# Kernel tuning notes

Measured on AMD Instinct MI355X. Metric: run time of the kernel, lower is better.

## Reference

```python
import jax, jax.numpy as jnp
import numpy as np

D = 256          # in_dim == out_dim for both layers
B, S = 8, 1024   # batch, seq_len
EPS = 1e-5       # LayerNorm eps (torch default)


def _layernorm(x, g, b):
    mu = jnp.mean(x, axis=-1, keepdims=True)
    var = jnp.var(x, axis=-1, keepdims=True)
    return (x - mu) * jax.lax.rsqrt(var + EPS) * g + b


def _periods(d):
    i = jnp.arange(d, dtype=jnp.float32)
    # periods[i, j] = i*d + j + 2
    return i[:, None] * d + i[None, :] + 2.0


def _layer(x, M, P, g, b, positions):
    # x: [B, S, in_dim] -> [B, S, out_dim]
    x_trans = jnp.einsum('bsj,ij->bsi', x, M)      # x @ M.T
    x_trans = _layernorm(x_trans, g, b)
    k = positions.astype(jnp.float32)[:, None, None]            # [S,1,1]
    phi = jnp.cos(2.0 * jnp.pi * k / _periods(D)[None])         # [S,D,D]
    Mk = P[None] * phi                                          # [S,D,D]
    Nk = jnp.einsum('bsj,sij->bsi', x_trans, Mk)
    # use_residual='separate' with in_dim==out_dim -> Identity residual
    return Nk + x


def setup_inputs() -> dict:
    key = jax.random.key(0)
    ks = jax.random.split(key, 5)
    seq = jax.random.normal(ks[0], (B, S, D), dtype=jnp.float32)
    M1 = jax.random.uniform(ks[1], (D, D), jnp.float32, -0.5, 0.5)
    P1 = jax.random.uniform(ks[2], (D, D), jnp.float32, -0.1, 0.1)
    M2 = jax.random.uniform(ks[3], (D, D), jnp.float32, -0.5, 0.5)
    P2 = jax.random.uniform(ks[4], (D, D), jnp.float32, -0.1, 0.1)
    g1 = jnp.ones((D,), jnp.float32); b1 = jnp.zeros((D,), jnp.float32)
    g2 = jnp.ones((D,), jnp.float32); b2 = jnp.zeros((D,), jnp.float32)
    return {"seq": seq, "M1": M1, "P1": P1, "g1": g1, "b1": b1,
            "M2": M2, "P2": P2, "g2": g2, "b2": b2}


def reference(seq, M1, P1, g1, b1, M2, P2, g2, b2):
    positions = jnp.arange(S)
    x = _layer(seq, M1, P1, g1, b1, positions)
    x = _layer(x, M2, P2, g2, b2, positions)
    return x
```

## Files before the change

kernel.cpp:

```cpp
#include <hip/hip_runtime.h>

#define DD 256
#define BB 8
#define SS 1024
#define XSTRIDE 264

#define LAYER_BYTES 524288
#define PTAB_OFF    131072
#define ITAB_OFF    262144
#define WS_NEEDED   (2 * LAYER_BYTES)

typedef _Float16 half8  __attribute__((ext_vector_type(8)));
typedef _Float16 half2t __attribute__((ext_vector_type(2)));
typedef __fp16   fp16x2 __attribute__((ext_vector_type(2)));
typedef __attribute__((ext_vector_type(4))) float float4v;

__device__ __forceinline__ half2t pkrtz(float a, float b) {
    union { fp16x2 f; half2t h; } cv;
    cv.f = __builtin_amdgcn_cvt_pkrtz(a, b);
    return cv.h;
}

__global__ void build_tabs(const float* __restrict__ M1, const float* __restrict__ P1,
                           const float* __restrict__ M2, const float* __restrict__ P2,
                           char* __restrict__ ws)
{
    int gid   = blockIdx.x * 256 + threadIdx.x;
    int layer = gid >> 13;
    int gi    = gid & 8191;
    int idx   = gi >> 6;
    int lane  = gi & 63;
    int kt    = idx >> 4;
    int wt    = idx & 15;
    int l15   = lane & 15, quad = lane >> 4;
    int n     = 16 * wt + l15;
    int j0    = kt * 32 + quad * 8;

    const float* Msrc = layer ? M2 : M1;
    const float* Psrc = layer ? P2 : P1;

    union { half8 h; half2t h2[4]; } mh, ph;
    float iv[8];
    #pragma unroll
    for (int e = 0; e < 4; ++e) {
        float ma = Msrc[(size_t)n * DD + j0 + 2 * e];
        float mb = Msrc[(size_t)n * DD + j0 + 2 * e + 1];
        float pa = Psrc[(size_t)n * DD + j0 + 2 * e];
        float pb = Psrc[(size_t)n * DD + j0 + 2 * e + 1];
        mh.h2[e] = pkrtz(ma, mb);
        ph.h2[e] = pkrtz(pa, pb);
        iv[2 * e]     = 1.0f / (float)(n * DD + j0 + 2 * e + 2);
        iv[2 * e + 1] = 1.0f / (float)(n * DD + j0 + 2 * e + 3);
    }
    char* base = ws + (size_t)layer * LAYER_BYTES;
    ((half8*)base)[gi]                       = mh.h;
    ((half8*)(base + PTAB_OFF))[gi]          = ph.h;
    float4* it = (float4*)(base + ITAB_OFF);
    it[2 * gi]     = make_float4(iv[0], iv[1], iv[2], iv[3]);
    it[2 * gi + 1] = make_float4(iv[4], iv[5], iv[6], iv[7]);
}

template<bool TABS>
__global__ __launch_bounds__(512, 4)
void fused_hierddpm(const float* __restrict__ seq,
                    const float* __restrict__ M1, const float* __restrict__ P1,
                    const float* __restrict__ g1, const float* __restrict__ be1,
                    const float* __restrict__ M2, const float* __restrict__ P2,
                    const float* __restrict__ g2, const float* __restrict__ be2,
                    const char* __restrict__ ws,
                    float* __restrict__ out)
{
    __shared__ __align__(16) _Float16 xsb[16][XSTRIDE];
    __shared__ __align__(16) _Float16 xtb[16][XSTRIDE];
    __shared__ float stats[8][16][2];

    const int tid  = threadIdx.x;
    const int w    = tid >> 6;
    const int lane = tid & 63;
    const int l15  = lane & 15;
    const int quad = lane >> 4;
    const int s0   = blockIdx.x * 2;
    const float k0 = (float)s0, k1 = (float)(s0 + 1);

    {
        const float4* seq4 = (const float4*)seq;
        #pragma unroll
        for (int u = 0; u < 2; ++u) {
            int v  = tid + 512 * u;
            int sl = v >> 9;
            int rm = v & 511;
            int b  = rm >> 6, j4 = rm & 63;
            float4 x = seq4[((size_t)b * SS + s0 + sl) * 64 + j4];
            half2t* dst = (half2t*)&xsb[sl * 8 + b][4 * j4];
            dst[0] = pkrtz(x.x, x.y);
            dst[1] = pkrtz(x.z, x.w);
        }
    }

    float res[2][4];
    {
        const int sl = quad >> 1;
        #pragma unroll
        for (int t = 0; t < 2; ++t) {
            int col = 16 * (2 * w + t) + l15;
            #pragma unroll
            for (int reg = 0; reg < 4; ++reg) {
                int b = (quad * 4 + reg) & 7;
                res[t][reg] = seq[((size_t)b * SS + s0 + sl) * DD + col];
            }
        }
    }
    __syncthreads();

    #pragma unroll 1
    for (int layer = 0; layer < 2; ++layer) {
        const float* M  = layer ? M2  : M1;
        const float* P  = layer ? P2  : P1;
        const float* g  = layer ? g2  : g1;
        const float* be = layer ? be2 : be1;
        const char*  lbase = ws + (size_t)layer * LAYER_BYTES;
        const half8*  Mtab = (const half8*)lbase;
        const half8*  Ptab = (const half8*)(lbase + PTAB_OFF);
        const float4* Itab = (const float4*)(lbase + ITAB_OFF);

        float4v acc1[2];
        acc1[0] = (float4v){0.f, 0.f, 0.f, 0.f};
        acc1[1] = (float4v){0.f, 0.f, 0.f, 0.f};

        #pragma unroll 1
        for (int kt = 0; kt < 8; ++kt) {
            half8 a = *(const half8*)&xsb[l15][kt * 32 + quad * 8];
            #pragma unroll
            for (int t = 0; t < 2; ++t) {
                half8 bfrag;
                if (TABS) {
                    bfrag = Mtab[(kt * 16 + 2 * w + t) * 64 + lane];
                } else {
                    int n = 16 * (2 * w + t) + l15;
                    const float4* Mr = (const float4*)M +
                        ((size_t)n * 64 + kt * 8 + quad * 2);
                    float4 m0 = Mr[0], m1 = Mr[1];
                    union { half8 h; half2t h2[4]; } bb;
                    bb.h2[0] = pkrtz(m0.x, m0.y);
                    bb.h2[1] = pkrtz(m0.z, m0.w);
                    bb.h2[2] = pkrtz(m1.x, m1.y);
                    bb.h2[3] = pkrtz(m1.z, m1.w);
                    bfrag = bb.h;
                }
                acc1[t] = __builtin_amdgcn_mfma_f32_16x16x32_f16(a, bfrag, acc1[t], 0, 0, 0);
            }
        }

        {
            #pragma unroll
            for (int reg = 0; reg < 4; ++reg) {
                float sm = acc1[0][reg] + acc1[1][reg];
                float sq = fmaf(acc1[0][reg], acc1[0][reg], acc1[1][reg] * acc1[1][reg]);
                #pragma unroll
                for (int off = 1; off < 16; off <<= 1) {
                    sm += __shfl_xor(sm, off, 64);
                    sq += __shfl_xor(sq, off, 64);
                }
                if (l15 == 0) {
                    stats[w][quad * 4 + reg][0] = sm;
                    stats[w][quad * 4 + reg][1] = sq;
                }
            }
        }
        __syncthreads();
        {
            float mu[4], rs[4];
            #pragma unroll
            for (int reg = 0; reg < 4; ++reg) {
                int m = quad * 4 + reg;
                float sm = 0.f, sq = 0.f;
                #pragma unroll
                for (int ww = 0; ww < 8; ++ww) {
                    sm += stats[ww][m][0];
                    sq += stats[ww][m][1];
                }
                float mm = sm * (1.f / DD);
                mu[reg] = mm;
                rs[reg] = rsqrtf(sq * (1.f / DD) - mm * mm + 1e-5f);
            }
            #pragma unroll
            for (int t = 0; t < 2; ++t) {
                int col = 16 * (2 * w + t) + l15;
                float gv = g[col], bv = be[col];
                #pragma unroll
                for (int reg = 0; reg < 4; ++reg) {
                    float v = fmaf((acc1[t][reg] - mu[reg]) * rs[reg], gv, bv);
                    xtb[quad * 4 + reg][col] = (_Float16)v;
                }
            }
        }
        __syncthreads();

        float4v accS[2][2];
        #pragma unroll
        for (int sl = 0; sl < 2; ++sl)
            #pragma unroll
            for (int t = 0; t < 2; ++t) accS[sl][t] = (float4v){0.f, 0.f, 0.f, 0.f};

        #pragma unroll 2
        for (int kt = 0; kt < 8; ++kt) {
            half8 a = *(const half8*)&xtb[l15][kt * 32 + quad * 8];
            #pragma unroll
            for (int t = 0; t < 2; ++t) {
                union { half8 h; half2t h2[4]; } pv;
                float iv[8];
                if (TABS) {
                    int gi = (kt * 16 + 2 * w + t) * 64 + lane;
                    pv.h = Ptab[gi];
                    float4 i0 = Itab[2 * gi], i1 = Itab[2 * gi + 1];
                    iv[0] = i0.x; iv[1] = i0.y; iv[2] = i0.z; iv[3] = i0.w;
                    iv[4] = i1.x; iv[5] = i1.y; iv[6] = i1.z; iv[7] = i1.w;
                } else {
                    int n = 16 * (2 * w + t) + l15;
                    const float4* Pr = (const float4*)P +
                        ((size_t)n * 64 + kt * 8 + quad * 2);
                    float4 p0 = Pr[0], p1 = Pr[1];
                    pv.h2[0] = pkrtz(p0.x, p0.y);
                    pv.h2[1] = pkrtz(p0.z, p0.w);
                    pv.h2[2] = pkrtz(p1.x, p1.y);
                    pv.h2[3] = pkrtz(p1.z, p1.w);
                    float pbase = (float)(n * DD + kt * 32 + quad * 8 + 2);
                    #pragma unroll
                    for (int e = 0; e < 8; ++e)
                        iv[e] = __builtin_amdgcn_rcpf(pbase + (float)e);
                }
                union { half8 h; half2t h2[4]; } b0, b1;
                #pragma unroll
                for (int e = 0; e < 4; ++e) {
                    float ia = iv[2 * e], ib = iv[2 * e + 1];
                    half2t c0 = pkrtz(
                        __builtin_amdgcn_cosf(__builtin_amdgcn_fractf(k0 * ia)),
                        __builtin_amdgcn_cosf(__builtin_amdgcn_fractf(k0 * ib)));
                    half2t c1 = pkrtz(
                        __builtin_amdgcn_cosf(__builtin_amdgcn_fractf(k1 * ia)),
                        __builtin_amdgcn_cosf(__builtin_amdgcn_fractf(k1 * ib)));
                    b0.h2[e] = pv.h2[e] * c0;
                    b1.h2[e] = pv.h2[e] * c1;
                }
                accS[0][t] = __builtin_amdgcn_mfma_f32_16x16x32_f16(a, b0.h, accS[0][t], 0, 0, 0);
                accS[1][t] = __builtin_amdgcn_mfma_f32_16x16x32_f16(a, b1.h, accS[1][t], 0, 0, 0);
            }
        }

        #pragma unroll
        for (int t = 0; t < 2; ++t) {
            int col = 16 * (2 * w + t) + l15;
            float4v av = (quad < 2) ? accS[0][t] : accS[1][t];
            int sl = quad >> 1;
            #pragma unroll
            for (int reg = 0; reg < 4; ++reg) {
                int m = quad * 4 + reg;
                int b = m & 7;
                float val = av[reg] + res[t][reg];
                if (layer == 0) {
                    res[t][reg] = val;
                    xsb[m][col] = (_Float16)val;
                } else {
                    out[((size_t)b * SS + s0 + sl) * DD + col] = val;
                }
            }
        }
        if (layer == 0) __syncthreads();
    }
}

extern "C" void kernel_launch(void* const* d_in, const int* in_sizes, int n_in,
                              void* d_out, int out_size, void* d_ws, size_t ws_size,
                              hipStream_t stream)
{
    const float* seq = (const float*)d_in[0];
    const float* M1  = (const float*)d_in[1];
    const float* P1  = (const float*)d_in[2];
    const float* g1  = (const float*)d_in[3];
    const float* b1  = (const float*)d_in[4];
    const float* M2  = (const float*)d_in[5];
    const float* P2  = (const float*)d_in[6];
    const float* g2  = (const float*)d_in[7];
    const float* b2  = (const float*)d_in[8];
    float* out = (float*)d_out;

    if (ws_size >= WS_NEEDED) {
        build_tabs<<<64, 256, 0, stream>>>(M1, P1, M2, P2, (char*)d_ws);
        fused_hierddpm<true><<<SS / 2, 512, 0, stream>>>(
            seq, M1, P1, g1, b1, M2, P2, g2, b2, (const char*)d_ws, out);
    } else {
        fused_hierddpm<false><<<SS / 2, 512, 0, stream>>>(
            seq, M1, P1, g1, b1, M2, P2, g2, b2, nullptr, out);
    }
}
```

Before: 114.4 us.

## Replace per-element cosines with second-order angle-difference expansion from one sincos

```diff
diff --git a/kernel.cpp b/kernel.cpp
--- a/kernel.cpp
+++ b/kernel.cpp
@@ -7,8 +7,11 @@
 
 #define LAYER_BYTES 524288
 #define PTAB_OFF    131072
-#define ITAB_OFF    262144
+#define JTAB_OFF    262144
 #define WS_NEEDED   (2 * LAYER_BYTES)
+
+#define TWO_PI 6.28318530717958647692f
+#define PBMIN  640.0f
 
 typedef _Float16 half8  __attribute__((ext_vector_type(8)));
 typedef _Float16 half2t __attribute__((ext_vector_type(2)));
@@ -40,24 +43,26 @@
     const float* Psrc = layer ? P2 : P1;
 
     union { half8 h; half2t h2[4]; } mh, ph;
-    float iv[8];
     #pragma unroll
     for (int e = 0; e < 4; ++e) {
-        float ma = Msrc[(size_t)n * DD + j0 + 2 * e];
-        float mb = Msrc[(size_t)n * DD + j0 + 2 * e + 1];
-        float pa = Psrc[(size_t)n * DD + j0 + 2 * e];
-        float pb = Psrc[(size_t)n * DD + j0 + 2 * e + 1];
-        mh.h2[e] = pkrtz(ma, mb);
-        ph.h2[e] = pkrtz(pa, pb);
-        iv[2 * e]     = 1.0f / (float)(n * DD + j0 + 2 * e + 2);
-        iv[2 * e + 1] = 1.0f / (float)(n * DD + j0 + 2 * e + 3);
-    }
+        mh.h2[e] = pkrtz(Msrc[(size_t)n * DD + j0 + 2 * e],
+                         Msrc[(size_t)n * DD + j0 + 2 * e + 1]);
+        ph.h2[e] = pkrtz(Psrc[(size_t)n * DD + j0 + 2 * e],
+                         Psrc[(size_t)n * DD + j0 + 2 * e + 1]);
+    }
+    float p0 = (float)(n * DD + j0 + 2);
+    float dv[8];
+    dv[0] = 1.0f / p0;
+    #pragma unroll
+    for (int e = 1; e < 8; ++e)
+        dv[e] = TWO_PI * (float)e / (p0 * (p0 + (float)e));
+
     char* base = ws + (size_t)layer * LAYER_BYTES;
-    ((half8*)base)[gi]                       = mh.h;
-    ((half8*)(base + PTAB_OFF))[gi]          = ph.h;
-    float4* it = (float4*)(base + ITAB_OFF);
-    it[2 * gi]     = make_float4(iv[0], iv[1], iv[2], iv[3]);
-    it[2 * gi + 1] = make_float4(iv[4], iv[5], iv[6], iv[7]);
+    ((half8*)base)[gi]              = mh.h;
+    ((half8*)(base + PTAB_OFF))[gi] = ph.h;
+    float4* jt = (float4*)(base + JTAB_OFF);
+    jt[2 * gi]     = make_float4(dv[0], dv[1], dv[2], dv[3]);
+    jt[2 * gi + 1] = make_float4(dv[4], dv[5], dv[6], dv[7]);
 }
 
 template<bool TABS>
@@ -121,13 +126,13 @@
         const char*  lbase = ws + (size_t)layer * LAYER_BYTES;
         const half8*  Mtab = (const half8*)lbase;
         const half8*  Ptab = (const half8*)(lbase + PTAB_OFF);
-        const float4* Itab = (const float4*)(lbase + ITAB_OFF);
+        const float4* Jtab = (const float4*)(lbase + JTAB_OFF);
 
         float4v acc1[2];
         acc1[0] = (float4v){0.f, 0.f, 0.f, 0.f};
         acc1[1] = (float4v){0.f, 0.f, 0.f, 0.f};
 
-        #pragma unroll 1
+        #pragma unroll 2
         for (int kt = 0; kt < 8; ++kt) {
             half8 a = *(const half8*)&xsb[l15][kt * 32 + quad * 8];
             #pragma unroll
@@ -207,40 +212,61 @@
             half8 a = *(const half8*)&xtb[l15][kt * 32 + quad * 8];
             #pragma unroll
             for (int t = 0; t < 2; ++t) {
-                union { half8 h; half2t h2[4]; } pv;
-                float iv[8];
+                const int n = 16 * (2 * w + t) + l15;
+                const float p0f = (float)(n * DD + kt * 32 + quad * 8 + 2);
+                union { half8 h; half2t h2[4]; } pv, b0, b1;
+
                 if (TABS) {
                     int gi = (kt * 16 + 2 * w + t) * 64 + lane;
                     pv.h = Ptab[gi];
-                    float4 i0 = Itab[2 * gi], i1 = Itab[2 * gi + 1];
-                    iv[0] = i0.x; iv[1] = i0.y; iv[2] = i0.z; iv[3] = i0.w;
-                    iv[4] = i1.x; iv[5] = i1.y; iv[6] = i1.z; iv[7] = i1.w;
+                    float4 ja = Jtab[2 * gi], jb = Jtab[2 * gi + 1];
+                    const float iv0 = ja.x;
+                    float f0 = __builtin_amdgcn_fractf(k0 * iv0);
+                    float c0 = __builtin_amdgcn_cosf(f0);
+                    float s0v = __builtin_amdgcn_sinf(f0);
+                    float dl = TWO_PI * iv0;
+                    float c1 = fmaf(-dl, fmaf(0.5f * dl, c0, s0v), c0);
+                    float s1v = fmaf(dl, fmaf(-0.5f * dl, s0v, c0), s0v);
+                    const float dd[8] = {0.f, ja.y, ja.z, ja.w, jb.x, jb.y, jb.z, jb.w};
+                    #pragma unroll
+                    for (int ep = 0; ep < 4; ++ep) {
+                        float da = dd[2 * ep], db = dd[2 * ep + 1];
+                        float pa0 = k0 * da, pb0 = k0 * db;
+                        float ce0a = fmaf(pa0, fmaf(-0.5f * pa0, c0, s0v), c0);
+                        float ce0b = fmaf(pb0, fmaf(-0.5f * pb0, c0, s0v), c0);
+                        float pa1 = k1 * da, pb1 = k1 * db;
+                        float ce1a = fmaf(pa1, fmaf(-0.5f * pa1, c1, s1v), c1);
+                        float ce1b = fmaf(pb1, fmaf(-0.5f * pb1, c1, s1v), c1);
+                        if (p0f < PBMIN) {
+                            float ia = __builtin_amdgcn_rcpf(p0f + (float)(2 * ep));
+                            float ib = __builtin_amdgcn_rcpf(p0f + (float)(2 * ep + 1));
+                            ce0a = __builtin_amdgcn_cosf(__builtin_amdgcn_fractf(k0 * ia));
+                            ce0b = __builtin_amdgcn_cosf(__builtin_amdgcn_fractf(k0 * ib));
+                            ce1a = __builtin_amdgcn_cosf(__builtin_amdgcn_fractf(k1 * ia));
+                            ce1b = __builtin_amdgcn_cosf(__builtin_amdgcn_fractf(k1 * ib));
+                        }
+                        b0.h2[ep] = pv.h2[ep] * pkrtz(ce0a, ce0b);
+                        b1.h2[ep] = pv.h2[ep] * pkrtz(ce1a, ce1b);
+                    }
                 } else {
-                    int n = 16 * (2 * w + t) + l15;
                     const float4* Pr = (const float4*)P +
                         ((size_t)n * 64 + kt * 8 + quad * 2);
-                    float4 p0 = Pr[0], p1 = Pr[1];
-                    pv.h2[0] = pkrtz(p0.x, p0.y);
-                    pv.h2[1] = pkrtz(p0.z, p0.w);
-                    pv.h2[2] = pkrtz(p1.x, p1.y);
-                    pv.h2[3] = pkrtz(p1.z, p1.w);
-                    float pbase = (float)(n * DD + kt * 32 + quad * 8 + 2);
+                    float4 q0 = Pr[0], q1 = Pr[1];
+                    pv.h2[0] = pkrtz(q0.x, q0.y);
+                    pv.h2[1] = pkrtz(q0.z, q0.w);
+                    pv.h2[2] = pkrtz(q1.x, q1.y);
+                    pv.h2[3] = pkrtz(q1.z, q1.w);
                     #pragma unroll
-                    for (int e = 0; e < 8; ++e)
-                        iv[e] = __builtin_amdgcn_rcpf(pbase + (float)e);
-                }
-                union { half8 h; half2t h2[4]; } b0, b1;
-                #pragma unroll
-                for (int e = 0; e < 4; ++e) {
-                    float ia = iv[2 * e], ib = iv[2 * e + 1];
-                    half2t c0 = pkrtz(
-                        __builtin_amdgcn_cosf(__builtin_amdgcn_fractf(k0 * ia)),
-                        __builtin_amdgcn_cosf(__builtin_amdgcn_fractf(k0 * ib)));
-                    half2t c1 = pkrtz(
-                        __builtin_amdgcn_cosf(__builtin_amdgcn_fractf(k1 * ia)),
-                        __builtin_amdgcn_cosf(__builtin_amdgcn_fractf(k1 * ib)));
-                    b0.h2[e] = pv.h2[e] * c0;
-                    b1.h2[e] = pv.h2[e] * c1;
+                    for (int ep = 0; ep < 4; ++ep) {
+                        float ia = __builtin_amdgcn_rcpf(p0f + (float)(2 * ep));
+                        float ib = __builtin_amdgcn_rcpf(p0f + (float)(2 * ep + 1));
+                        float ce0a = __builtin_amdgcn_cosf(__builtin_amdgcn_fractf(k0 * ia));
+                        float ce0b = __builtin_amdgcn_cosf(__builtin_amdgcn_fractf(k0 * ib));
+                        float ce1a = __builtin_amdgcn_cosf(__builtin_amdgcn_fractf(k1 * ia));
+                        float ce1b = __builtin_amdgcn_cosf(__builtin_amdgcn_fractf(k1 * ib));
+                        b0.h2[ep] = pv.h2[ep] * pkrtz(ce0a, ce0b);
+                        b1.h2[ep] = pv.h2[ep] * pkrtz(ce1a, ce1b);
+                    }
                 }
                 accS[0][t] = __builtin_amdgcn_mfma_f32_16x16x32_f16(a, b0.h, accS[0][t], 0, 0, 0);
                 accS[1][t] = __builtin_amdgcn_mfma_f32_16x16x32_f16(a, b1.h, accS[1][t], 0, 0, 0);
```

After: 118.2 us. 3.3% more time.
